# Performance work log

Hardware: AMD Instinct MI355X
Metric: run time of the kernel (lower is better)

The kernel has to match this reference:

```python
import jax, jax.numpy as jnp
import numpy as np

COMMITMENT = 0.25

def setup_inputs() -> dict:
    key = jax.random.key(0)
    k1, k2 = jax.random.split(key)
    x = jax.random.normal(k1, (64, 256, 32, 32), dtype=jnp.float32)
    embed = jax.random.normal(k2, (256, 1024), dtype=jnp.float32)  # [emb_dim, num_emb]
    return {"x": x, "embed": embed}

def reference(x, embed):
    # x: [B, C, H, W] -> NHWC
    xt = jnp.transpose(x, (0, 2, 3, 1))              # [B, H, W, C]
    B, H, W, C = xt.shape
    flat = xt.reshape(-1, C)                         # [N, C]
    # squared euclidean distances to each codebook column
    dist = (jnp.sum(flat * flat, axis=1, keepdims=True)
            - 2.0 * flat @ embed
            + jnp.sum(embed * embed, axis=0, keepdims=True))  # [N, num_emb]
    embed_idx = jnp.argmin(dist, axis=1).reshape(B, H, W)     # [B, H, W]
    quantize = embed.T[embed_idx]                    # [B, H, W, C]
    e_latent_loss = jnp.mean((jax.lax.stop_gradient(quantize) - xt) ** 2)
    q_latent_loss = jnp.mean((quantize - jax.lax.stop_gradient(xt)) ** 2)
    loss = q_latent_loss + COMMITMENT * e_latent_loss
    # straight-through estimator
    quantize = xt + jax.lax.stop_gradient(quantize - xt)
    quantize = jnp.transpose(quantize, (0, 3, 1, 2))  # back to NCHW
    return quantize, loss, embed_idx
```

## Files before the change

### kernel.cpp

```cpp
#include <hip/hip_runtime.h>

#define CDIM 256
#define HW   1024
#define NPIX 65536
#define KDIM 1024
#define TAU  0.5f
#define RB   8
#define SWZ(c) (((c) & 31) ^ (((c) >> 3) & 24))

using bf16x8 = __attribute__((ext_vector_type(8))) short;
using f32x4  = __attribute__((ext_vector_type(4))) float;
typedef unsigned int u32;

static __device__ __forceinline__ unsigned short f2bf(float v) {
    union { float f; unsigned u; } a; a.f = v;
    unsigned u = a.u;
    u += 0x7fffu + ((u >> 16) & 1u);
    return (unsigned short)(u >> 16);
}

static __device__ __forceinline__ void gload_lds16(const void* g, void* s) {
    __builtin_amdgcn_global_load_lds(
        (const __attribute__((address_space(1))) u32*)g,
        (__attribute__((address_space(3))) u32*)s,
        16, 0, 0);
}

__global__ void ee_kernel(const float* __restrict__ embed, float* __restrict__ ee) {
    int k = blockIdx.x * 256 + threadIdx.x;
    float s = 0.f;
#pragma unroll 8
    for (int c = 0; c < CDIM; ++c) {
        float v = embed[c * KDIM + k];
        s += v * v;
    }
    ee[k] = s;
}

__global__ void transpose_e(const float* __restrict__ embed, float* __restrict__ embedT) {
    __shared__ float tl[32][33];
    const int t = threadIdx.x;
    const int j = t & 31, r = t >> 5;
    const int k0 = (blockIdx.x & 31) * 32;
    const int c0 = (blockIdx.x >> 5) * 32;
#pragma unroll
    for (int rr = 0; rr < 4; ++rr) {
        int c = r * 4 + rr;
        tl[c][j] = embed[(size_t)(c0 + c) * KDIM + k0 + j];
    }
    __syncthreads();
#pragma unroll
    for (int rr = 0; rr < 4; ++rr) {
        int k = r * 4 + rr;
        embedT[(size_t)(k0 + k) * CDIM + c0 + j] = tl[j][k];
    }
}

__global__ void prep_e(const float* __restrict__ embed, short* __restrict__ e_hi) {
    int tid = blockIdx.x * 256 + threadIdx.x;
    int l  = tid & 63;
    int f  = tid >> 6;
    int nf = f & 3;
    int ks = (f >> 2) & 7;
    int nh = (f >> 5) & 1;
    int nt = f >> 6;
    int n  = nt * 128 + (nh * 4 + nf) * 16 + (l & 15);
    int c0 = ks * 32 + (l >> 4) * 8;
    bf16x8 h8;
#pragma unroll
    for (int j = 0; j < 8; ++j)
        h8[j] = (short)f2bf(-2.0f * embed[(c0 + j) * KDIM + n]);
    *(bf16x8*)&e_hi[(size_t)tid * 8] = h8;
}

__launch_bounds__(256, 3)
__global__ void vq_gemm(const float* __restrict__ x, const short* __restrict__ e_hi,
                        const float* __restrict__ ee,
                        float* __restrict__ hv1, float* __restrict__ hv2,
                        int* __restrict__ hidx) {
    __shared__ short Bs[2][8192];
    const int t  = threadIdx.x;
    const int l  = t & 63;
    const int w  = t >> 6;
    const int lr = l & 15;
    const int lg = l >> 4;
    const int tile    = blockIdx.x & 511;
    const int quarter = blockIdx.x >> 9;
    const int px0 = tile * 128 + w * 32;
    const int b   = px0 >> 10;
    const int p0  = px0 & 1023;
    const float* xb = x + (size_t)b * CDIM * HW;

    const int c_first = quarter * 8;
    {
        const int slab = w * 4;
        const char* srcb = (const char*)e_hi +
            (size_t)(((c_first >> 2) * 2 + ((c_first >> 1) & 1)) * 32 + (c_first & 1) * 2) * 1024 + l * 16;
        char* dstb = (char*)&Bs[0][0] + (size_t)slab * 1024 + l * 16;
#pragma unroll
        for (int i = 0; i < 4; ++i) {
            int s = slab + i;
            gload_lds16(srcb + (size_t)((s >> 1) * 4 + (s & 1)) * 1024, dstb + (size_t)i * 1024);
        }
    }

    bf16x8 a[2][8];
#pragma unroll
    for (int mf = 0; mf < 2; ++mf) {
#pragma unroll
        for (int ks = 0; ks < 8; ++ks) {
            const float* p = xb + (size_t)(ks * 32 + lg * 8) * HW + p0 + mf * 16 + lr;
            float v[8];
#pragma unroll
            for (int j = 0; j < 8; ++j) v[j] = p[(size_t)j * HW];
#pragma unroll
            for (int j = 0; j < 8; ++j) a[mf][ks][j] = (short)f2bf(v[j]);
        }
    }

    float minv[8], min2v[8];
    int   mini[8];
#pragma unroll
    for (int r = 0; r < 8; ++r) { minv[r] = 3.4e38f; min2v[r] = 3.4e38f; mini[r] = 0; }

    __syncthreads();

    for (int cc = 0; cc < 8; ++cc) {
        const int c   = c_first + cc;
        const int cur = cc & 1;
        if (cc < 7) {
            const int cn = c + 1;
            const int slab = w * 4;
            const char* srcb = (const char*)e_hi +
                (size_t)(((cn >> 2) * 2 + ((cn >> 1) & 1)) * 32 + (cn & 1) * 2) * 1024 + l * 16;
            char* dstb = (char*)&Bs[cur ^ 1][0] + (size_t)slab * 1024 + l * 16;
#pragma unroll
            for (int i = 0; i < 4; ++i) {
                int s = slab + i;
                gload_lds16(srcb + (size_t)((s >> 1) * 4 + (s & 1)) * 1024, dstb + (size_t)i * 1024);
            }
        }

        f32x4 acc[2][2];
#pragma unroll
        for (int mf = 0; mf < 2; ++mf)
#pragma unroll
            for (int nfi = 0; nfi < 2; ++nfi)
                acc[mf][nfi] = (f32x4){0.f, 0.f, 0.f, 0.f};

#pragma unroll
        for (int ks = 0; ks < 8; ++ks) {
#pragma unroll
            for (int nfi = 0; nfi < 2; ++nfi) {
                bf16x8 bh = *(const bf16x8*)&Bs[cur][((ks * 2 + nfi) * 64 + l) * 8];
#pragma unroll
                for (int mf = 0; mf < 2; ++mf)
                    acc[mf][nfi] = __builtin_amdgcn_mfma_f32_16x16x32_bf16(a[mf][ks], bh, acc[mf][nfi], 0, 0, 0);
            }
        }

#pragma unroll
        for (int nfi = 0; nfi < 2; ++nfi) {
            const int kg = c * 32 + nfi * 16 + lr;
            const float eev = ee[kg];
#pragma unroll
            for (int mf = 0; mf < 2; ++mf)
#pragma unroll
                for (int j = 0; j < 4; ++j) {
                    const int r = mf * 4 + j;
                    float m = acc[mf][nfi][j] + eev;
                    bool lt = m < minv[r];
                    float sec = lt ? minv[r] : m;
                    minv[r] = lt ? m : minv[r];
                    mini[r] = lt ? kg : mini[r];
                    min2v[r] = fminf(min2v[r], sec);
                }
        }
        __syncthreads();
    }

#pragma unroll
    for (int r = 0; r < 8; ++r) {
        float v1 = minv[r]; int i1 = mini[r]; float v2 = min2v[r];
#pragma unroll
        for (int mask = 1; mask < 16; mask <<= 1) {
            float ov1 = __shfl_xor(v1, mask, 64);
            int   oi1 = __shfl_xor(i1, mask, 64);
            float ov2 = __shfl_xor(v2, mask, 64);
            float vmax = fmaxf(v1, ov1);
            v2 = fminf(fminf(v2, ov2), vmax);
            bool take = (ov1 < v1) || (ov1 == v1 && oi1 < i1);
            v1 = take ? ov1 : v1;
            i1 = take ? oi1 : i1;
        }
        if (lr == 0) {
            int px = px0 + (r >> 2) * 16 + lg * 4 + (r & 3);
            int o = quarter * NPIX + px;
            hv1[o] = v1; hv2[o] = v2; hidx[o] = i1;
        }
    }
}

__global__ void merge_quarters(const float* __restrict__ hv1, const float* __restrict__ hv2,
                               const int* __restrict__ hidx, int* __restrict__ idx_out,
                               int* __restrict__ worklist, int* __restrict__ wcount) {
    int px = blockIdx.x * 256 + threadIdx.x;
    float v1 = hv1[px], v2 = hv2[px];
    int   i1 = hidx[px];
#pragma unroll
    for (int q = 1; q < 4; ++q) {
        float va = hv1[q * NPIX + px];
        float sa = hv2[q * NPIX + px];
        int   ia = hidx[q * NPIX + px];
        if (va < v1) {
            v2 = fminf(v1, sa);
            v1 = va; i1 = ia;
        } else {
            v2 = fminf(v2, va);
        }
    }
    idx_out[px] = i1;
    if (v2 - v1 < TAU) {
        int pos = atomicAdd(wcount, 1);
        worklist[pos] = px;
    }
}

__launch_bounds__(256)
__global__ void vq_rescue(const float* __restrict__ x, const float* __restrict__ embed,
                          const float* __restrict__ ee,
                          const int* __restrict__ worklist, const int* __restrict__ wcount,
                          int* __restrict__ idx_out) {
    __shared__ float xs[RB][CDIM];
    __shared__ int   pxs[RB];
    __shared__ float redv[4][RB];
    __shared__ int   redi[4][RB];
    const int t  = threadIdx.x;
    const int wv = t >> 6, ln = t & 63;
    const int cnt = *wcount;
    for (int base = blockIdx.x * RB; base < cnt; base += gridDim.x * RB) {
        const int nb = min(RB, cnt - base);
        __syncthreads();
        if (t < RB) pxs[t] = worklist[base + (t < nb ? t : nb - 1)];
        __syncthreads();
#pragma unroll
        for (int i = 0; i < RB; ++i) {
            int gn = pxs[i];
            xs[i][t] = x[(size_t)(gn >> 10) * CDIM * HW + (size_t)t * HW + (gn & 1023)];
        }
        __syncthreads();

        float4 acc[RB];
#pragma unroll
        for (int i = 0; i < RB; ++i) acc[i] = make_float4(0.f, 0.f, 0.f, 0.f);
#pragma unroll 4
        for (int c = 0; c < CDIM; ++c) {
            float4 ev = *(const float4*)&embed[c * KDIM + t * 4];
#pragma unroll
            for (int i = 0; i < RB; ++i) {
                float xv = xs[i][c];
                acc[i].x = fmaf(xv, ev.x, acc[i].x);
                acc[i].y = fmaf(xv, ev.y, acc[i].y);
                acc[i].z = fmaf(xv, ev.z, acc[i].z);
                acc[i].w = fmaf(xv, ev.w, acc[i].w);
            }
        }
        const float4 eev = *(const float4*)&ee[t * 4];
#pragma unroll
        for (int i = 0; i < RB; ++i) {
            float d0 = fmaf(-2.f, acc[i].x, eev.x);
            float d1 = fmaf(-2.f, acc[i].y, eev.y);
            float d2 = fmaf(-2.f, acc[i].z, eev.z);
            float d3 = fmaf(-2.f, acc[i].w, eev.w);
            float v = d0; int ix = t * 4;
            if (d1 < v) { v = d1; ix = t * 4 + 1; }
            if (d2 < v) { v = d2; ix = t * 4 + 2; }
            if (d3 < v) { v = d3; ix = t * 4 + 3; }
#pragma unroll
            for (int mask = 1; mask < 64; mask <<= 1) {
                float ov = __shfl_xor(v, mask, 64);
                int   oi = __shfl_xor(ix, mask, 64);
                bool take = (ov < v) || (ov == v && oi < ix);
                v = take ? ov : v; ix = take ? oi : ix;
            }
            if (ln == 0) { redv[wv][i] = v; redi[wv][i] = ix; }
        }
        __syncthreads();
        if (t < nb) {
            float fv = redv[0][t]; int fi = redi[0][t];
#pragma unroll
            for (int q = 1; q < 4; ++q) {
                float v = redv[q][t]; int ix = redi[q][t];
                if (v < fv || (v == fv && ix < fi)) { fv = v; fi = ix; }
            }
            idx_out[pxs[t]] = fi;
        }
    }
}

__launch_bounds__(256)
__global__ void vq_epilogue(const float* __restrict__ x, const float* __restrict__ embed,
                            const float* __restrict__ embedT, int useT,
                            const int* __restrict__ idx_in, float* __restrict__ out_q,
                            float* __restrict__ out_idx, float* __restrict__ partials) {
    __shared__ float q[16384];
    __shared__ int   idxs[128];
    __shared__ float lred[4];
    const int t = threadIdx.x;
    const int w = t >> 6, l = t & 63;
    const int n0 = blockIdx.x * 128;
    const int b  = n0 >> 10;

    if (t < 128) idxs[t] = idx_in[n0 + t];
    __syncthreads();
    if (t < 128) out_idx[n0 + t] = (float)idxs[t];

    const int j  = t >> 2;
    const int qd = t & 3;
    float lsum = 0.f;

#pragma unroll
    for (int pass = 0; pass < 2; ++pass) {
        const int myidx = idxs[pass * 64 + j];
        if (useT) {
            const float4* src4 = (const float4*)embedT + (size_t)myidx * 64;
#pragma unroll
            for (int i = 0; i < 16; ++i) {
                float4 v = src4[qd * 16 + i];
                int c = qd * 64 + i * 4;
                q[(c + 0) * 64 + (j ^ SWZ(c + 0))] = v.x;
                q[(c + 1) * 64 + (j ^ SWZ(c + 1))] = v.y;
                q[(c + 2) * 64 + (j ^ SWZ(c + 2))] = v.z;
                q[(c + 3) * 64 + (j ^ SWZ(c + 3))] = v.w;
            }
        } else {
#pragma unroll 4
            for (int i = 0; i < 64; ++i) {
                int c = qd * 64 + i;
                q[c * 64 + (j ^ SWZ(c))] = embed[(size_t)c * KDIM + myidx];
            }
        }
        __syncthreads();

        const int p0 = (n0 & 1023) + pass * 64;
        const size_t xbase = (size_t)b * CDIM * HW + p0;
#pragma unroll 8
        for (int ci = 0; ci < 64; ++ci) {
            int c = w * 64 + ci;
            float qv = q[c * 64 + (l ^ SWZ(c))];
            float xv = x[xbase + (size_t)c * HW + l];
            out_q[xbase + (size_t)c * HW + l] = qv;
            float d = qv - xv;
            lsum = fmaf(d, d, lsum);
        }
        __syncthreads();
    }

#pragma unroll
    for (int off = 32; off > 0; off >>= 1)
        lsum += __shfl_down(lsum, off, 64);
    if (l == 0) lred[w] = lsum;
    __syncthreads();
    if (t == 0)
        partials[blockIdx.x] = (lred[0] + lred[1]) + (lred[2] + lred[3]);
}

__global__ void loss_kernel(const float* __restrict__ partials, float* __restrict__ out_loss) {
    __shared__ float s[256];
    s[threadIdx.x] = partials[threadIdx.x] + partials[threadIdx.x + 256];
    __syncthreads();
    for (int off = 128; off > 0; off >>= 1) {
        if (threadIdx.x < off) s[threadIdx.x] += s[threadIdx.x + off];
        __syncthreads();
    }
    if (threadIdx.x == 0)
        out_loss[0] = 1.25f * s[0] / 16777216.0f;
}

extern "C" void kernel_launch(void* const* d_in, const int* in_sizes, int n_in,
                              void* d_out, int out_size, void* d_ws, size_t ws_size,
                              hipStream_t stream) {
    const float* x     = (const float*)d_in[0];
    const float* embed = (const float*)d_in[1];
    float* out_q    = (float*)d_out;
    float* out_loss = out_q + (size_t)NPIX * CDIM;
    float* out_idx  = out_loss + 1;
    int*   idx_i32  = (int*)out_idx;

    short* e_hi     = (short*)out_q;
    int*   worklist = (int*)(out_q + 131072);
    float* hv1      = out_q + 196608;
    float* hv2      = out_q + 458752;
    int*   hidx     = (int*)(out_q + 720896);

    float* ws       = (float*)d_ws;
    float* ee       = ws;
    int*   wcount   = (int*)(ws + 1024);
    float* partials = ws + 1088;
    float* embedT   = ws + 1600;
    int useT = (ws_size >= (size_t)(1600 + 262144) * sizeof(float)) ? 1 : 0;

    ee_kernel<<<KDIM / 256, 256, 0, stream>>>(embed, ee);
    if (useT) transpose_e<<<256, 256, 0, stream>>>(embed, embedT);
    prep_e<<<128, 256, 0, stream>>>(embed, e_hi);
    hipMemsetAsync(wcount, 0, 4, stream);
    vq_gemm<<<2048, 256, 0, stream>>>(x, e_hi, ee, hv1, hv2, hidx);
    merge_quarters<<<NPIX / 256, 256, 0, stream>>>(hv1, hv2, hidx, idx_i32, worklist, wcount);
    vq_rescue<<<2048, 256, 0, stream>>>(x, embed, ee, worklist, wcount, idx_i32);
    vq_epilogue<<<NPIX / 128, 256, 0, stream>>>(x, embed, useT ? embedT : embed, useT,
                                                idx_i32, out_q, out_idx, partials);
    loss_kernel<<<1, 256, 0, stream>>>(partials, out_loss);
}
```

Before: 181.1 us.

## Drop codebook split across blocks; scan full codebook per tile and fuse merge

The GEMM kernel no longer splits the 1024-entry codebook into four quarters across separate blocks. Each block now loops over all 32 codebook chunks for its 128 pixels and writes the final index and rescue worklist entry directly. This removes the merge_quarters kernel and the intermediate hv1/hv2/hidx traffic, and each block loads its activation tile once instead of four times. The cost is a grid cut from 2048 to 512 blocks, which reduces parallelism on a large GPU, and the occupancy hint drops to 2 blocks per SM.

```diff
diff --git a/kernel.cpp b/kernel.cpp
--- a/kernel.cpp
+++ b/kernel.cpp
@@ -73,29 +73,24 @@
     *(bf16x8*)&e_hi[(size_t)tid * 8] = h8;
 }
 
-__launch_bounds__(256, 3)
+__launch_bounds__(256, 2)
 __global__ void vq_gemm(const float* __restrict__ x, const short* __restrict__ e_hi,
-                        const float* __restrict__ ee,
-                        float* __restrict__ hv1, float* __restrict__ hv2,
-                        int* __restrict__ hidx) {
+                        const float* __restrict__ ee, int* __restrict__ idx_out,
+                        int* __restrict__ worklist, int* __restrict__ wcount) {
     __shared__ short Bs[2][8192];
     const int t  = threadIdx.x;
     const int l  = t & 63;
     const int w  = t >> 6;
     const int lr = l & 15;
     const int lg = l >> 4;
-    const int tile    = blockIdx.x & 511;
-    const int quarter = blockIdx.x >> 9;
-    const int px0 = tile * 128 + w * 32;
+    const int px0 = blockIdx.x * 128 + w * 32;
     const int b   = px0 >> 10;
     const int p0  = px0 & 1023;
     const float* xb = x + (size_t)b * CDIM * HW;
 
-    const int c_first = quarter * 8;
     {
         const int slab = w * 4;
-        const char* srcb = (const char*)e_hi +
-            (size_t)(((c_first >> 2) * 2 + ((c_first >> 1) & 1)) * 32 + (c_first & 1) * 2) * 1024 + l * 16;
+        const char* srcb = (const char*)e_hi + (size_t)l * 16;
         char* dstb = (char*)&Bs[0][0] + (size_t)slab * 1024 + l * 16;
 #pragma unroll
         for (int i = 0; i < 4; ++i) {
@@ -125,10 +120,9 @@
 
     __syncthreads();
 
-    for (int cc = 0; cc < 8; ++cc) {
-        const int c   = c_first + cc;
-        const int cur = cc & 1;
-        if (cc < 7) {
+    for (int c = 0; c < 32; ++c) {
+        const int cur = c & 1;
+        if (c < 31) {
             const int cn = c + 1;
             const int slab = w * 4;
             const char* srcb = (const char*)e_hi +
@@ -195,34 +189,12 @@
         }
         if (lr == 0) {
             int px = px0 + (r >> 2) * 16 + lg * 4 + (r & 3);
-            int o = quarter * NPIX + px;
-            hv1[o] = v1; hv2[o] = v2; hidx[o] = i1;
-        }
-    }
-}
-
-__global__ void merge_quarters(const float* __restrict__ hv1, const float* __restrict__ hv2,
-                               const int* __restrict__ hidx, int* __restrict__ idx_out,
-                               int* __restrict__ worklist, int* __restrict__ wcount) {
-    int px = blockIdx.x * 256 + threadIdx.x;
-    float v1 = hv1[px], v2 = hv2[px];
-    int   i1 = hidx[px];
-#pragma unroll
-    for (int q = 1; q < 4; ++q) {
-        float va = hv1[q * NPIX + px];
-        float sa = hv2[q * NPIX + px];
-        int   ia = hidx[q * NPIX + px];
-        if (va < v1) {
-            v2 = fminf(v1, sa);
-            v1 = va; i1 = ia;
-        } else {
-            v2 = fminf(v2, va);
-        }
-    }
-    idx_out[px] = i1;
-    if (v2 - v1 < TAU) {
-        int pos = atomicAdd(wcount, 1);
-        worklist[pos] = px;
+            idx_out[px] = i1;
+            if (v2 - v1 < TAU) {
+                int pos = atomicAdd(wcount, 1);
+                worklist[pos] = px;
+            }
+        }
     }
 }
 
@@ -389,9 +361,6 @@
 
     short* e_hi     = (short*)out_q;
     int*   worklist = (int*)(out_q + 131072);
-    float* hv1      = out_q + 196608;
-    float* hv2      = out_q + 458752;
-    int*   hidx     = (int*)(out_q + 720896);
 
     float* ws       = (float*)d_ws;
     float* ee       = ws;
@@ -404,8 +373,7 @@
     if (useT) transpose_e<<<256, 256, 0, stream>>>(embed, embedT);
     prep_e<<<128, 256, 0, stream>>>(embed, e_hi);
     hipMemsetAsync(wcount, 0, 4, stream);
-    vq_gemm<<<2048, 256, 0, stream>>>(x, e_hi, ee, hv1, hv2, hidx);
-    merge_quarters<<<NPIX / 256, 256, 0, stream>>>(hv1, hv2, hidx, idx_i32, worklist, wcount);
+    vq_gemm<<<NPIX / 128, 256, 0, stream>>>(x, e_hi, ee, idx_i32, worklist, wcount);
     vq_rescue<<<2048, 256, 0, stream>>>(x, embed, ee, worklist, wcount, idx_i32);
     vq_epilogue<<<NPIX / 128, 256, 0, stream>>>(x, embed, useT ? embedT : embed, useT,
                                                 idx_i32, out_q, out_idx, partials);
```

Result: faster. 171.3 us (-5.4%).
